# Performance work log

Measured on AMD Instinct MI355X. Metric: run time of the kernel, lower is better.

The kernel has to match this reference:

```python
import jax, jax.numpy as jnp
import numpy as np

N_NODES = 100000
IN_C = 512
OUT_C = 128
ITERATIONS = 3
NNZ_FEAT = 2_000_000
N_EDGES = 1_600_000


def setup_inputs() -> dict:
    key = jax.random.key(0)
    k1, k2, k3, k4, k5, k6, k7 = jax.random.split(key, 7)
    # sparse feature matrix: COO indices [2, nnz] (row in [0,N_NODES), col in [0,IN_C))
    f_rows = jax.random.randint(k1, (NNZ_FEAT,), 0, N_NODES)
    f_cols = jax.random.randint(k2, (NNZ_FEAT,), 0, IN_C)
    # force the max indices to be present so feature_count == (N_NODES, IN_C)
    f_rows = f_rows.at[-1].set(N_NODES - 1)
    f_cols = f_cols.at[-1].set(IN_C - 1)
    feat_indices = jnp.stack([f_rows, f_cols]).astype(jnp.int64)
    feat_values = jax.random.uniform(k3, (NNZ_FEAT,), dtype=jnp.float32)
    # sparse normalized adjacency: COO indices [2, n_edges]
    a_rows = jax.random.randint(k4, (N_EDGES,), 0, N_NODES)
    a_cols = jax.random.randint(k5, (N_EDGES,), 0, N_NODES)
    adj_indices = jnp.stack([a_rows, a_cols]).astype(jnp.int64)
    # normalized weights ~ 1/degree scale
    adj_values = jax.random.uniform(k6, (N_EDGES,), dtype=jnp.float32) / 16.0
    # learned parameters (xavier-uniform style scale)
    wb = float(np.sqrt(6.0 / (IN_C + OUT_C)))
    weight = jax.random.uniform(k7, (IN_C, OUT_C), minval=-wb, maxval=wb, dtype=jnp.float32)
    bias = jax.random.uniform(jax.random.fold_in(key, 99), (1, OUT_C), minval=-wb, maxval=wb, dtype=jnp.float32)
    return {
        "feat_indices": feat_indices,
        "feat_values": feat_values,
        "adj_indices": adj_indices,
        "adj_values": adj_values,
        "weight": weight,
        "bias": bias,
    }


def reference(feat_indices, feat_values, adj_indices, adj_values, weight, bias):
    # spmm(feat_indices, feat_values, N, IN_C, weight): sparse [N, IN_C] @ dense [IN_C, OUT_C]
    f_rows, f_cols = feat_indices[0], feat_indices[1]
    msgs = feat_values[:, None] * weight[f_cols]              # [nnz, OUT_C]
    base = jax.ops.segment_sum(msgs, f_rows, num_segments=N_NODES)  # [N, OUT_C]
    base = base + bias
    # dropout in eval mode (training=False) is identity
    base = jax.nn.relu(base)
    a_rows, a_cols = adj_indices[0], adj_indices[1]
    for _ in range(ITERATIONS - 1):
        # sparse [N, N] @ dense [N, OUT_C]
        base = jax.ops.segment_sum(adj_values[:, None] * base[a_cols], a_rows, num_segments=N_NODES)
    return base
```

## Files before the change

kernel.cpp:

```cpp
#include <hip/hip_runtime.h>

#define N_NODES 100000
#define VROWS   200000
#define BSHIFT  8
#define BROWS   256
#define NBUCK   ((VROWS + BROWS - 1) / BROWS)
#define BINB    256

static __device__ __forceinline__ unsigned short f2bf(float x) {
    unsigned u = __float_as_uint(x);
    return (unsigned short)((u + 0x7fffu + ((u >> 16) & 1u)) >> 16);
}
static __device__ __forceinline__ float bf_lo(unsigned u) { return __uint_as_float(u << 16); }
static __device__ __forceinline__ float bf_hi(unsigned u) { return __uint_as_float(u & 0xffff0000u); }

static __device__ __forceinline__ void nt_colval(const long long* p, int& c, float& v) {
    long long e = __builtin_nontemporal_load(p);
    c = (int)(e & 0x1ffffLL);
    v = __uint_as_float((unsigned)((unsigned long long)e >> 32));
}

static __device__ __forceinline__ long long pack_cv(int col, int rl, float v) {
    unsigned lo = (unsigned)col | ((unsigned)rl << 17);
    return (long long)lo | ((long long)(unsigned)__float_as_uint(v) << 32);
}


__global__ void zero_small_kernel(int* __restrict__ p, int n) {
    int i = blockIdx.x * blockDim.x + threadIdx.x;
    if (i < n) p[i] = 0;
}

__global__ __launch_bounds__(256) void binA_kernel(
        const int* __restrict__ f_rows, const int* __restrict__ a_rows,
        int* __restrict__ cur, int* __restrict__ pbb, int nnzf, int nedge) {
    __shared__ int hist[NBUCK];
    const int t = threadIdx.x;
    for (int b = t; b < NBUCK; b += 256) hist[b] = 0;
    __syncthreads();
    {
        const int per = (nnzf + BINB - 1) / BINB;
        const int beg = blockIdx.x * per;
        const int end = min(beg + per, nnzf);
        int i = beg + t;
        for (; i + 3 * 256 < end; i += 4 * 256) {
            int r0 = f_rows[i], r1 = f_rows[i + 256], r2 = f_rows[i + 512], r3 = f_rows[i + 768];
            atomicAdd(&hist[r0 >> BSHIFT], 1);
            atomicAdd(&hist[r1 >> BSHIFT], 1);
            atomicAdd(&hist[r2 >> BSHIFT], 1);
            atomicAdd(&hist[r3 >> BSHIFT], 1);
        }
        for (; i < end; i += 256) atomicAdd(&hist[f_rows[i] >> BSHIFT], 1);
    }
    {
        const int per = (nedge + BINB - 1) / BINB;
        const int beg = blockIdx.x * per;
        const int end = min(beg + per, nedge);
        int i = beg + t;
        for (; i + 3 * 256 < end; i += 4 * 256) {
            int r0 = a_rows[i] + N_NODES, r1 = a_rows[i + 256] + N_NODES;
            int r2 = a_rows[i + 512] + N_NODES, r3 = a_rows[i + 768] + N_NODES;
            atomicAdd(&hist[r0 >> BSHIFT], 1);
            atomicAdd(&hist[r1 >> BSHIFT], 1);
            atomicAdd(&hist[r2 >> BSHIFT], 1);
            atomicAdd(&hist[r3 >> BSHIFT], 1);
        }
        for (; i < end; i += 256) atomicAdd(&hist[(a_rows[i] + N_NODES) >> BSHIFT], 1);
    }
    __syncthreads();
    for (int b = t; b < NBUCK; b += 256) {
        int c = hist[b];
        pbb[blockIdx.x * NBUCK + b] = c ? atomicAdd(&cur[b], c) : 0;
    }
}

__global__ void bucket_scan_kernel(const int* __restrict__ cur, int* __restrict__ bbase,
                                   int* __restrict__ rp) {
    __shared__ int sh[1024];
    const int t = threadIdx.x;
    int v = (t < NBUCK) ? cur[t] : 0;
    sh[t] = v;
    __syncthreads();
    for (int off = 1; off < 1024; off <<= 1) {
        int u = (t >= off) ? sh[t - off] : 0;
        __syncthreads();
        sh[t] += u;
        __syncthreads();
    }
    if (t < NBUCK) bbase[t] = sh[t] - v;
    if (t == NBUCK - 1) rp[VROWS] = sh[t];
}

__global__ __launch_bounds__(256) void binB_kernel(
        const int* __restrict__ f_rows, const int* __restrict__ f_cols, const float* __restrict__ f_vals,
        const int* __restrict__ a_rows, const int* __restrict__ a_cols, const float* __restrict__ a_vals,
        const int* __restrict__ bbase, const int* __restrict__ pbb,
        long long* __restrict__ staging, int nnzf, int nedge) {
    __shared__ int curs[NBUCK];
    const int t = threadIdx.x;
    for (int b = t; b < NBUCK; b += 256) curs[b] = bbase[b] + pbb[blockIdx.x * NBUCK + b];
    __syncthreads();
    {
        const int per = (nnzf + BINB - 1) / BINB;
        const int beg = blockIdx.x * per;
        const int end = min(beg + per, nnzf);
        for (int i = beg + t; i < end; i += 256) {
            const int   r = f_rows[i];
            const int   c = f_cols[i];
            const float v = f_vals[i];
            const int p = atomicAdd(&curs[r >> BSHIFT], 1);
            staging[p] = pack_cv(c, r & (BROWS - 1), v);
        }
    }
    {
        const int per = (nedge + BINB - 1) / BINB;
        const int beg = blockIdx.x * per;
        const int end = min(beg + per, nedge);
        for (int i = beg + t; i < end; i += 256) {
            const int   r = a_rows[i] + N_NODES;
            const int   c = a_cols[i];
            const float v = a_vals[i];
            const int p = atomicAdd(&curs[r >> BSHIFT], 1);
            staging[p] = pack_cv(c, r & (BROWS - 1), v);
        }
    }
}

__global__ __launch_bounds__(256) void sort_kernel(
        const int* __restrict__ cur, const int* __restrict__ bbase,
        const long long* __restrict__ staging, long long* __restrict__ colval,
        int* __restrict__ rp) {
    const int b = blockIdx.x;
    const int t = threadIdx.x;
    __shared__ int cnt[BROWS];
    __shared__ int offs[BROWS];
    cnt[t] = 0;
    __syncthreads();
    const int n = cur[b];
    const int base = bbase[b];
    const long long* seg = staging + base;
    for (int j = t; j < n; j += 256) {
        unsigned lo = (unsigned)(seg[j] & 0xffffffffLL);
        atomicAdd(&cnt[(lo >> 17) & (BROWS - 1)], 1);
    }
    __syncthreads();
    int v = cnt[t];
    offs[t] = v;
    __syncthreads();
    for (int o = 1; o < BROWS; o <<= 1) {
        int u = (t >= o) ? offs[t - o] : 0;
        __syncthreads();
        offs[t] += u;
        __syncthreads();
    }
    const int excl = offs[t] - v;
    offs[t] = base + excl;
    const int row = (b << BSHIFT) + t;
    if (row < VROWS) rp[row] = base + excl;
    __syncthreads();
    for (int j = t; j < n; j += 256) {
        long long e = seg[j];
        unsigned lo = (unsigned)(e & 0xffffffffLL);
        const int rl = (lo >> 17) & (BROWS - 1);
        const int p = atomicAdd(&offs[rl], 1);
        colval[p] = (long long)(lo & 0x1ffffu) | (e & 0xffffffff00000000LL);
    }
}


__global__ __launch_bounds__(256) void spmm_feat_kernel(
        const int* __restrict__ row_ptr, const long long* __restrict__ colval,
        const float* __restrict__ W, const float* __restrict__ bias,
        unsigned short* __restrict__ base_bf, int n) {
    const int wave = (blockIdx.x * blockDim.x + threadIdx.x) >> 6;
    const int lane = threadIdx.x & 63;
    const int h = lane >> 5;
    const int s = lane & 31;
    const int r = wave * 2 + h;
    const float4* __restrict__ W4 = (const float4*)W;
    float4 a0 = make_float4(0.f, 0.f, 0.f, 0.f), a1 = a0;
    int i = 0, end = 0;
    if (r < n) { i = row_ptr[r]; end = row_ptr[r + 1]; }
    for (; i + 1 < end; i += 2) {
        int c0, c1; float v0, v1;
        nt_colval(colval + i,     c0, v0);
        nt_colval(colval + i + 1, c1, v1);
        const float4 w0 = W4[c0 * 32 + s];
        const float4 w1 = W4[c1 * 32 + s];
        a0.x += v0 * w0.x; a0.y += v0 * w0.y; a0.z += v0 * w0.z; a0.w += v0 * w0.w;
        a1.x += v1 * w1.x; a1.y += v1 * w1.y; a1.z += v1 * w1.z; a1.w += v1 * w1.w;
    }
    if (i < end) {
        int c; float v;
        nt_colval(colval + i, c, v);
        const float4 w = W4[c * 32 + s];
        a0.x += v * w.x; a0.y += v * w.y; a0.z += v * w.z; a0.w += v * w.w;
    }
    if (r < n) {
        const float4 b = ((const float4*)bias)[s];
        ushort4 o;
        o.x = f2bf(fmaxf(a0.x + a1.x + b.x, 0.f));
        o.y = f2bf(fmaxf(a0.y + a1.y + b.y, 0.f));
        o.z = f2bf(fmaxf(a0.z + a1.z + b.z, 0.f));
        o.w = f2bf(fmaxf(a0.w + a1.w + b.w, 0.f));
        ((ushort4*)(base_bf + (size_t)r * 128))[s] = o;
    }
}


__global__ __launch_bounds__(256) void spmm_adj_bf_bf_kernel(
        const int* __restrict__ row_ptr, const long long* __restrict__ colval,
        const uint2* __restrict__ src, unsigned short* __restrict__ dst, int n) {
    const int wave = (blockIdx.x * blockDim.x + threadIdx.x) >> 6;
    const int lane = threadIdx.x & 63;
    const int h = lane >> 5;
    const int s = lane & 31;
    const int r = wave * 2 + h;
    float4 a0 = make_float4(0.f, 0.f, 0.f, 0.f), a1 = a0;
    int i = 0, end = 0;
    if (r < n) { i = row_ptr[r]; end = row_ptr[r + 1]; }
    for (; i + 1 < end; i += 2) {
        int c0, c1; float v0, v1;
        nt_colval(colval + i,     c0, v0);
        nt_colval(colval + i + 1, c1, v1);
        const uint2 u0 = src[c0 * 32 + s];
        const uint2 u1 = src[c1 * 32 + s];
        a0.x += v0 * bf_lo(u0.x); a0.y += v0 * bf_hi(u0.x);
        a0.z += v0 * bf_lo(u0.y); a0.w += v0 * bf_hi(u0.y);
        a1.x += v1 * bf_lo(u1.x); a1.y += v1 * bf_hi(u1.x);
        a1.z += v1 * bf_lo(u1.y); a1.w += v1 * bf_hi(u1.y);
    }
    if (i < end) {
        int c; float v;
        nt_colval(colval + i, c, v);
        const uint2 u = src[c * 32 + s];
        a0.x += v * bf_lo(u.x); a0.y += v * bf_hi(u.x);
        a0.z += v * bf_lo(u.y); a0.w += v * bf_hi(u.y);
    }
    if (r < n) {
        ushort4 o;
        o.x = f2bf(a0.x + a1.x); o.y = f2bf(a0.y + a1.y);
        o.z = f2bf(a0.z + a1.z); o.w = f2bf(a0.w + a1.w);
        ((ushort4*)(dst + (size_t)r * 128))[s] = o;
    }
}


__global__ __launch_bounds__(256) void spmm_adj_bf_f32_kernel(
        const int* __restrict__ row_ptr, const long long* __restrict__ colval,
        const uint2* __restrict__ src, float* __restrict__ dst, int n) {
    const int wave = (blockIdx.x * blockDim.x + threadIdx.x) >> 6;
    const int lane = threadIdx.x & 63;
    const int h = lane >> 5;
    const int s = lane & 31;
    const int r = wave * 2 + h;
    float4 a0 = make_float4(0.f, 0.f, 0.f, 0.f), a1 = a0;
    int i = 0, end = 0;
    if (r < n) { i = row_ptr[r]; end = row_ptr[r + 1]; }
    for (; i + 1 < end; i += 2) {
        int c0, c1; float v0, v1;
        nt_colval(colval + i,     c0, v0);
        nt_colval(colval + i + 1, c1, v1);
        const uint2 u0 = src[c0 * 32 + s];
        const uint2 u1 = src[c1 * 32 + s];
        a0.x += v0 * bf_lo(u0.x); a0.y += v0 * bf_hi(u0.x);
        a0.z += v0 * bf_lo(u0.y); a0.w += v0 * bf_hi(u0.y);
        a1.x += v1 * bf_lo(u1.x); a1.y += v1 * bf_hi(u1.x);
        a1.z += v1 * bf_lo(u1.y); a1.w += v1 * bf_hi(u1.y);
    }
    if (i < end) {
        int c; float v;
        nt_colval(colval + i, c, v);
        const uint2 u = src[c * 32 + s];
        a0.x += v * bf_lo(u.x); a0.y += v * bf_hi(u.x);
        a0.z += v * bf_lo(u.y); a0.w += v * bf_hi(u.y);
    }
    if (r < n) {
        float4 acc;
        acc.x = a0.x + a1.x; acc.y = a0.y + a1.y;
        acc.z = a0.z + a1.z; acc.w = a0.w + a1.w;
        ((float4*)(dst + (size_t)r * 128))[s] = acc;
    }
}


extern "C" void kernel_launch(void* const* d_in, const int* in_sizes, int n_in,
                              void* d_out, int out_size, void* d_ws, size_t ws_size,
                              hipStream_t stream) {
    const int*   fi   = (const int*)d_in[0];
    const float* fv   = (const float*)d_in[1];
    const int*   ai   = (const int*)d_in[2];
    const float* av   = (const float*)d_in[3];
    const float* W    = (const float*)d_in[4];
    const float* bias = (const float*)d_in[5];
    float* out = (float*)d_out;

    const int nnzf  = in_sizes[1];
    const int nedge = in_sizes[3];
    const int ntot  = nnzf + nedge;
    const int* f_rows = fi;
    const int* f_cols = fi + nnzf;
    const int* a_rows = ai;
    const int* a_cols = ai + nedge;

    char* wp = (char*)d_ws;
    auto balloc = [&](size_t bytes) -> char* {
        char* p = wp;
        wp += (bytes + 255) & ~(size_t)255;
        return p;
    };
    long long* staging = (long long*)balloc(8ull * (size_t)ntot);
    unsigned short* base_bf = (unsigned short*)staging;
    unsigned short* t1 = (unsigned short*)balloc(2ull * N_NODES * 128);
    long long* colval = (long long*)balloc(8ull * (size_t)ntot);
    int* rp    = (int*)balloc(4ull * (VROWS + 1));
    int* cur   = (int*)balloc(4ull * NBUCK);
    int* bbase = (int*)balloc(4ull * NBUCK);
    int* pbb   = (int*)balloc(4ull * BINB * NBUCK);

    const int nwaves = (N_NODES + 1) / 2;
    const int RW = (nwaves + 3) / 4;

    zero_small_kernel<<<(NBUCK + 255) / 256, 256, 0, stream>>>(cur, NBUCK);
    binA_kernel<<<BINB, 256, 0, stream>>>(f_rows, a_rows, cur, pbb, nnzf, nedge);
    bucket_scan_kernel<<<1, 1024, 0, stream>>>(cur, bbase, rp);
    binB_kernel<<<BINB, 256, 0, stream>>>(f_rows, f_cols, fv, a_rows, a_cols, av,
                                          bbase, pbb, staging, nnzf, nedge);
    sort_kernel<<<NBUCK, 256, 0, stream>>>(cur, bbase, staging, colval, rp);

    spmm_feat_kernel<<<RW, 256, 0, stream>>>(rp, colval, W, bias, base_bf, N_NODES);
    spmm_adj_bf_bf_kernel<<<RW, 256, 0, stream>>>(rp + N_NODES, colval,
                                                  (const uint2*)base_bf, t1, N_NODES);
    spmm_adj_bf_f32_kernel<<<RW, 256, 0, stream>>>(rp + N_NODES, colval,
                                                   (const uint2*)t1, out, N_NODES);
}
```

Before: 335.8 us.

## Process four rows per wave with 16-byte bf16 gathers and bf16 weight

Changes the SpMM kernels from two rows per wave, each lane gathering 8 bytes, to four rows per wave, each lane gathering 16 bytes (eight bf16 values). The dense weight is also converted to bf16 by a new small kernel, so the feature SpMM gathers half as many bytes per nonzero. This raises the number of independent row gathers in flight per wave and widens the memory transactions. In exchange it adds an extra launch, rounds the weight to bf16, and raises per-lane register use.

```diff
diff --git a/kernel.cpp b/kernel.cpp
--- a/kernel.cpp
+++ b/kernel.cpp
@@ -25,10 +25,25 @@
     return (long long)lo | ((long long)(unsigned)__float_as_uint(v) << 32);
 }
 
+static __device__ __forceinline__ void fma8(float4& lo, float4& hi, float v, const uint4& u) {
+    lo.x += v * bf_lo(u.x); lo.y += v * bf_hi(u.x);
+    lo.z += v * bf_lo(u.y); lo.w += v * bf_hi(u.y);
+    hi.x += v * bf_lo(u.z); hi.y += v * bf_hi(u.z);
+    hi.z += v * bf_lo(u.w); hi.w += v * bf_hi(u.w);
+}
+
 
 __global__ void zero_small_kernel(int* __restrict__ p, int n) {
     int i = blockIdx.x * blockDim.x + threadIdx.x;
     if (i < n) p[i] = 0;
+}
+
+__global__ void wconv_kernel(const float* __restrict__ W, unsigned* __restrict__ Wbf) {
+    int i = blockIdx.x * blockDim.x + threadIdx.x;
+    if (i < 512 * 64) {
+        float a = W[2 * i], b = W[2 * i + 1];
+        Wbf[i] = (unsigned)f2bf(a) | ((unsigned)f2bf(b) << 16);
+    }
 }
 
 __global__ __launch_bounds__(256) void binA_kernel(
@@ -168,118 +183,115 @@
 }
 
 
-__global__ __launch_bounds__(256) void spmm_feat_kernel(
-        const int* __restrict__ row_ptr, const long long* __restrict__ colval,
-        const float* __restrict__ W, const float* __restrict__ bias,
+__global__ __launch_bounds__(256) void spmm_feat_q_kernel(
+        const int* __restrict__ rp, const long long* __restrict__ colval,
+        const uint4* __restrict__ Wbf, const float* __restrict__ bias,
         unsigned short* __restrict__ base_bf, int n) {
     const int wave = (blockIdx.x * blockDim.x + threadIdx.x) >> 6;
     const int lane = threadIdx.x & 63;
-    const int h = lane >> 5;
-    const int s = lane & 31;
-    const int r = wave * 2 + h;
-    const float4* __restrict__ W4 = (const float4*)W;
-    float4 a0 = make_float4(0.f, 0.f, 0.f, 0.f), a1 = a0;
+    const int q = lane >> 4, ql = lane & 15;
+    const int r = wave * 4 + q;
+    float4 a0l = make_float4(0.f, 0.f, 0.f, 0.f), a0h = a0l, a1l = a0l, a1h = a0l;
     int i = 0, end = 0;
-    if (r < n) { i = row_ptr[r]; end = row_ptr[r + 1]; }
+    if (r < n) { i = rp[r]; end = rp[r + 1]; }
     for (; i + 1 < end; i += 2) {
         int c0, c1; float v0, v1;
         nt_colval(colval + i,     c0, v0);
         nt_colval(colval + i + 1, c1, v1);
-        const float4 w0 = W4[c0 * 32 + s];
-        const float4 w1 = W4[c1 * 32 + s];
-        a0.x += v0 * w0.x; a0.y += v0 * w0.y; a0.z += v0 * w0.z; a0.w += v0 * w0.w;
-        a1.x += v1 * w1.x; a1.y += v1 * w1.y; a1.z += v1 * w1.z; a1.w += v1 * w1.w;
+        const uint4 u0 = Wbf[c0 * 16 + ql];
+        const uint4 u1 = Wbf[c1 * 16 + ql];
+        fma8(a0l, a0h, v0, u0);
+        fma8(a1l, a1h, v1, u1);
     }
     if (i < end) {
         int c; float v;
         nt_colval(colval + i, c, v);
-        const float4 w = W4[c * 32 + s];
-        a0.x += v * w.x; a0.y += v * w.y; a0.z += v * w.z; a0.w += v * w.w;
+        const uint4 u = Wbf[c * 16 + ql];
+        fma8(a0l, a0h, v, u);
     }
     if (r < n) {
-        const float4 b = ((const float4*)bias)[s];
-        ushort4 o;
-        o.x = f2bf(fmaxf(a0.x + a1.x + b.x, 0.f));
-        o.y = f2bf(fmaxf(a0.y + a1.y + b.y, 0.f));
-        o.z = f2bf(fmaxf(a0.z + a1.z + b.z, 0.f));
-        o.w = f2bf(fmaxf(a0.w + a1.w + b.w, 0.f));
-        ((ushort4*)(base_bf + (size_t)r * 128))[s] = o;
-    }
-}
-
-
-__global__ __launch_bounds__(256) void spmm_adj_bf_bf_kernel(
-        const int* __restrict__ row_ptr, const long long* __restrict__ colval,
-        const uint2* __restrict__ src, unsigned short* __restrict__ dst, int n) {
+        const float4 bl = ((const float4*)bias)[ql * 2];
+        const float4 bh = ((const float4*)bias)[ql * 2 + 1];
+        float s0 = fmaxf(a0l.x + a1l.x + bl.x, 0.f), s1 = fmaxf(a0l.y + a1l.y + bl.y, 0.f);
+        float s2 = fmaxf(a0l.z + a1l.z + bl.z, 0.f), s3 = fmaxf(a0l.w + a1l.w + bl.w, 0.f);
+        float s4 = fmaxf(a0h.x + a1h.x + bh.x, 0.f), s5 = fmaxf(a0h.y + a1h.y + bh.y, 0.f);
+        float s6 = fmaxf(a0h.z + a1h.z + bh.z, 0.f), s7 = fmaxf(a0h.w + a1h.w + bh.w, 0.f);
+        uint4 o;
+        o.x = (unsigned)f2bf(s0) | ((unsigned)f2bf(s1) << 16);
+        o.y = (unsigned)f2bf(s2) | ((unsigned)f2bf(s3) << 16);
+        o.z = (unsigned)f2bf(s4) | ((unsigned)f2bf(s5) << 16);
+        o.w = (unsigned)f2bf(s6) | ((unsigned)f2bf(s7) << 16);
+        ((uint4*)(base_bf + (size_t)r * 128))[ql] = o;
+    }
+}
+
+__global__ __launch_bounds__(256) void spmm_adj_q_bf_kernel(
+        const int* __restrict__ rp, const long long* __restrict__ colval,
+        const uint4* __restrict__ src, unsigned short* __restrict__ dst, int n) {
     const int wave = (blockIdx.x * blockDim.x + threadIdx.x) >> 6;
     const int lane = threadIdx.x & 63;
-    const int h = lane >> 5;
-    const int s = lane & 31;
-    const int r = wave * 2 + h;
-    float4 a0 = make_float4(0.f, 0.f, 0.f, 0.f), a1 = a0;
+    const int q = lane >> 4, ql = lane & 15;
+    const int r = wave * 4 + q;
+    float4 a0l = make_float4(0.f, 0.f, 0.f, 0.f), a0h = a0l, a1l = a0l, a1h = a0l;
     int i = 0, end = 0;
-    if (r < n) { i = row_ptr[r]; end = row_ptr[r + 1]; }
+    if (r < n) { i = rp[r]; end = rp[r + 1]; }
     for (; i + 1 < end; i += 2) {
         int c0, c1; float v0, v1;
         nt_colval(colval + i,     c0, v0);
         nt_colval(colval + i + 1, c1, v1);
-        const uint2 u0 = src[c0 * 32 + s];
-        const uint2 u1 = src[c1 * 32 + s];
-        a0.x += v0 * bf_lo(u0.x); a0.y += v0 * bf_hi(u0.x);
-        a0.z += v0 * bf_lo(u0.y); a0.w += v0 * bf_hi(u0.y);
-        a1.x += v1 * bf_lo(u1.x); a1.y += v1 * bf_hi(u1.x);
-        a1.z += v1 * bf_lo(u1.y); a1.w += v1 * bf_hi(u1.y);
+        const uint4 u0 = src[c0 * 16 + ql];
+        const uint4 u1 = src[c1 * 16 + ql];
+        fma8(a0l, a0h, v0, u0);
+        fma8(a1l, a1h, v1, u1);
     }
     if (i < end) {
         int c; float v;
         nt_colval(colval + i, c, v);
-        const uint2 u = src[c * 32 + s];
-        a0.x += v * bf_lo(u.x); a0.y += v * bf_hi(u.x);
-        a0.z += v * bf_lo(u.y); a0.w += v * bf_hi(u.y);
+        const uint4 u = src[c * 16 + ql];
+        fma8(a0l, a0h, v, u);
     }
     if (r < n) {
-        ushort4 o;
-        o.x = f2bf(a0.x + a1.x); o.y = f2bf(a0.y + a1.y);
-        o.z = f2bf(a0.z + a1.z); o.w = f2bf(a0.w + a1.w);
-        ((ushort4*)(dst + (size_t)r * 128))[s] = o;
-    }
-}
-
-
-__global__ __launch_bounds__(256) void spmm_adj_bf_f32_kernel(
-        const int* __restrict__ row_ptr, const long long* __restrict__ colval,
-        const uint2* __restrict__ src, float* __restrict__ dst, int n) {
+        uint4 o;
+        o.x = (unsigned)f2bf(a0l.x + a1l.x) | ((unsigned)f2bf(a0l.y + a1l.y) << 16);
+        o.y = (unsigned)f2bf(a0l.z + a1l.z) | ((unsigned)f2bf(a0l.w + a1l.w) << 16);
+        o.z = (unsigned)f2bf(a0h.x + a1h.x) | ((unsigned)f2bf(a0h.y + a1h.y) << 16);
+        o.w = (unsigned)f2bf(a0h.z + a1h.z) | ((unsigned)f2bf(a0h.w + a1h.w) << 16);
+        ((uint4*)(dst + (size_t)r * 128))[ql] = o;
+    }
+}
+
+__global__ __launch_bounds__(256) void spmm_adj_q_f32_kernel(
+        const int* __restrict__ rp, const long long* __restrict__ colval,
+        const uint4* __restrict__ src, float* __restrict__ dst, int n) {
     const int wave = (blockIdx.x * blockDim.x + threadIdx.x) >> 6;
     const int lane = threadIdx.x & 63;
-    const int h = lane >> 5;
-    const int s = lane & 31;
-    const int r = wave * 2 + h;
-    float4 a0 = make_float4(0.f, 0.f, 0.f, 0.f), a1 = a0;
+    const int q = lane >> 4, ql = lane & 15;
+    const int r = wave * 4 + q;
+    float4 a0l = make_float4(0.f, 0.f, 0.f, 0.f), a0h = a0l, a1l = a0l, a1h = a0l;
     int i = 0, end = 0;
-    if (r < n) { i = row_ptr[r]; end = row_ptr[r + 1]; }
+    if (r < n) { i = rp[r]; end = rp[r + 1]; }
     for (; i + 1 < end; i += 2) {
         int c0, c1; float v0, v1;
         nt_colval(colval + i,     c0, v0);
         nt_colval(colval + i + 1, c1, v1);
-        const uint2 u0 = src[c0 * 32 + s];
-        const uint2 u1 = src[c1 * 32 + s];
-        a0.x += v0 * bf_lo(u0.x); a0.y += v0 * bf_hi(u0.x);
-        a0.z += v0 * bf_lo(u0.y); a0.w += v0 * bf_hi(u0.y);
-        a1.x += v1 * bf_lo(u1.x); a1.y += v1 * bf_hi(u1.x);
-        a1.z += v1 * bf_lo(u1.y); a1.w += v1 * bf_hi(u1.y);
+        const uint4 u0 = src[c0 * 16 + ql];
+        const uint4 u1 = src[c1 * 16 + ql];
+        fma8(a0l, a0h, v0, u0);
+        fma8(a1l, a1h, v1, u1);
     }
     if (i < end) {
         int c; float v;
         nt_colval(colval + i, c, v);
-        const uint2 u = src[c * 32 + s];
-        a0.x += v * bf_lo(u.x); a0.y += v * bf_hi(u.x);
-        a0.z += v * bf_lo(u.y); a0.w += v * bf_hi(u.y);
+        const uint4 u = src[c * 16 + ql];
+        fma8(a0l, a0h, v, u);
     }
     if (r < n) {
-        float4 acc;
-        acc.x = a0.x + a1.x; acc.y = a0.y + a1.y;
-        acc.z = a0.z + a1.z; acc.w = a0.w + a1.w;
-        ((float4*)(dst + (size_t)r * 128))[s] = acc;
+        float4 lo, hi;
+        lo.x = a0l.x + a1l.x; lo.y = a0l.y + a1l.y; lo.z = a0l.z + a1l.z; lo.w = a0l.w + a1l.w;
+        hi.x = a0h.x + a1h.x; hi.y = a0h.y + a1h.y; hi.z = a0h.z + a1h.z; hi.w = a0h.w + a1h.w;
+        float4* dr = (float4*)(dst + (size_t)r * 128);
+        dr[ql * 2]     = lo;
+        dr[ql * 2 + 1] = hi;
     }
 }
 
@@ -313,24 +325,27 @@
     unsigned short* base_bf = (unsigned short*)staging;
     unsigned short* t1 = (unsigned short*)balloc(2ull * N_NODES * 128);
     long long* colval = (long long*)balloc(8ull * (size_t)ntot);
-    int* rp    = (int*)balloc(4ull * (VROWS + 1));
-    int* cur   = (int*)balloc(4ull * NBUCK);
-    int* bbase = (int*)balloc(4ull * NBUCK);
-    int* pbb   = (int*)balloc(4ull * BINB * NBUCK);
-
-    const int nwaves = (N_NODES + 1) / 2;
+    int* rp     = (int*)balloc(4ull * (VROWS + 1));
+    int* cur    = (int*)balloc(4ull * NBUCK);
+    int* bbase  = (int*)balloc(4ull * NBUCK);
+    int* pbb    = (int*)balloc(4ull * BINB * NBUCK);
+    unsigned* Wbf = (unsigned*)balloc(4ull * 512 * 64);
+
+    const int nwaves = (N_NODES + 3) / 4;
     const int RW = (nwaves + 3) / 4;
 
     zero_small_kernel<<<(NBUCK + 255) / 256, 256, 0, stream>>>(cur, NBUCK);
+    wconv_kernel<<<128, 256, 0, stream>>>(W, Wbf);
     binA_kernel<<<BINB, 256, 0, stream>>>(f_rows, a_rows, cur, pbb, nnzf, nedge);
     bucket_scan_kernel<<<1, 1024, 0, stream>>>(cur, bbase, rp);
     binB_kernel<<<BINB, 256, 0, stream>>>(f_rows, f_cols, fv, a_rows, a_cols, av,
                                           bbase, pbb, staging, nnzf, nedge);
     sort_kernel<<<NBUCK, 256, 0, stream>>>(cur, bbase, staging, colval, rp);
 
-    spmm_feat_kernel<<<RW, 256, 0, stream>>>(rp, colval, W, bias, base_bf, N_NODES);
-    spmm_adj_bf_bf_kernel<<<RW, 256, 0, stream>>>(rp + N_NODES, colval,
-                                                  (const uint2*)base_bf, t1, N_NODES);
-    spmm_adj_bf_f32_kernel<<<RW, 256, 0, stream>>>(rp + N_NODES, colval,
-                                                   (const uint2*)t1, out, N_NODES);
-}
+    spmm_feat_q_kernel<<<RW, 256, 0, stream>>>(rp, colval, (const uint4*)Wbf, bias,
+                                               base_bf, N_NODES);
+    spmm_adj_q_bf_kernel<<<RW, 256, 0, stream>>>(rp + N_NODES, colval,
+                                                 (const uint4*)base_bf, t1, N_NODES);
+    spmm_adj_q_f32_kernel<<<RW, 256, 0, stream>>>(rp + N_NODES, colval,
+                                                  (const uint4*)t1, out, N_NODES);
+}
```

After: 300.0 us. 1.12x faster.
